# Kernel tuning notes

Measured on AMD Instinct MI355X. Metric: run time of the kernel, lower is better.

The kernel has to match this reference:

```python
import jax, jax.numpy as jnp
import numpy as np

WH, WW = 7, 7
SH, SW = 3, 3
NUM_HEADS = 8


def _rel_pos_index(wh, ww):
    coords = np.stack(np.meshgrid(np.arange(wh), np.arange(ww), indexing='ij')).reshape(2, -1)
    rel = (coords[:, :, None] - coords[:, None, :]).transpose(1, 2, 0)  # [N,N,2]
    rel[..., 0] += wh - 1
    rel[..., 1] += ww - 1
    rel[..., 0] *= 2 * ww - 1
    return rel.sum(-1)  # [N,N] int


def _attn_mask(Hp, Wp, wh, ww, sh, sw):
    img = np.zeros((Hp, Wp), dtype=np.float32)
    cnt = 0
    for hs in (slice(0, -wh), slice(-wh, -sh), slice(-sh, None)):
        for ws in (slice(0, -ww), slice(-ww, -sw), slice(-sw, None)):
            img[hs, ws] = cnt
            cnt += 1
    win = img.reshape(Hp // wh, wh, Wp // ww, ww).transpose(0, 2, 1, 3).reshape(-1, wh * ww)  # [nW,N]
    diff = win[:, None, :] - win[:, :, None]  # [nW,N,N]
    return np.where(diff != 0, -100.0, 0.0).astype(np.float32)


def _layernorm(x, g, b, eps=1e-5):
    mu = jnp.mean(x, -1, keepdims=True)
    var = jnp.mean(jnp.square(x - mu), -1, keepdims=True)
    return (x - mu) * jax.lax.rsqrt(var + eps) * g + b


def setup_inputs() -> dict:
    key = jax.random.key(0)
    ks = jax.random.split(key, 12)
    B, H, W, C = 32, 56, 56, 256
    hid = 4 * C
    s = lambda k, *shape: jax.random.normal(k, shape, jnp.float32) * 0.02
    return {
        'x': jax.random.normal(ks[0], (B, H * W, C), jnp.float32),
        'g1': jnp.ones((C,), jnp.float32), 'b1': jnp.zeros((C,), jnp.float32),
        'qkv_w': s(ks[1], 3 * C, C), 'qkv_b': jnp.zeros((3 * C,), jnp.float32),
        'bias_table': s(ks[2], (2 * WH - 1) * (2 * WW - 1), NUM_HEADS),
        'proj_w': s(ks[3], C, C), 'proj_b': jnp.zeros((C,), jnp.float32),
        'g2': jnp.ones((C,), jnp.float32), 'b2': jnp.zeros((C,), jnp.float32),
        'w1': s(ks[4], hid, C), 'bm1': jnp.zeros((hid,), jnp.float32),
        'w2': s(ks[5], C, hid), 'bm2': jnp.zeros((C,), jnp.float32),
        'H': H, 'W': W,
    }


def reference(x, g1, b1, qkv_w, qkv_b, bias_table, proj_w, proj_b, g2, b2, w1, bm1, w2, bm2, H, W):
    B, L, C = x.shape
    wh, ww = WH, WW
    nH = NUM_HEADS
    hd = C // nH
    scale = hd ** -0.5
    N = wh * ww

    shortcut = x
    h = _layernorm(x, g1, b1).reshape(B, H, W, C)
    pad_b = (wh - H % wh) % wh
    pad_r = (ww - W % ww) % ww
    if pad_b or pad_r:
        h = jnp.pad(h, ((0, 0), (0, pad_b), (0, pad_r), (0, 0)))
    Hp, Wp = h.shape[1], h.shape[2]

    h = jnp.roll(h, (-SH, -SW), axis=(1, 2))
    # window partition -> [B*nW, N, C]
    nWh, nWw = Hp // wh, Wp // ww
    xw = h.reshape(B, nWh, wh, nWw, ww, C).transpose(0, 1, 3, 2, 4, 5).reshape(-1, N, C)

    qkv = jnp.einsum('bnc,oc->bno', xw, qkv_w) + qkv_b  # [B*nW, N, 3C]
    qkv = qkv.reshape(-1, N, 3, nH, hd).transpose(2, 0, 3, 1, 4)
    q, k, v = qkv[0] * scale, qkv[1], qkv[2]  # [B*nW, nH, N, hd]
    attn = jnp.einsum('whnd,whmd->whnm', q, k)  # [B*nW, nH, N, N]

    rpi = jnp.asarray(_rel_pos_index(wh, ww))
    bias = bias_table[rpi.reshape(-1)].reshape(N, N, nH).transpose(2, 0, 1)  # [nH,N,N]
    attn = attn + bias[None]

    mask = jnp.asarray(_attn_mask(Hp, Wp, wh, ww, SH, SW))  # [nW,N,N]
    nW = mask.shape[0]
    attn = attn.reshape(B, nW, nH, N, N) + mask[None, :, None]
    attn = jax.nn.softmax(attn.reshape(-1, nH, N, N), axis=-1)

    out = jnp.einsum('whnm,whmd->whnd', attn, v).transpose(0, 2, 1, 3).reshape(-1, N, C)
    out = jnp.einsum('bnc,oc->bno', out, proj_w) + proj_b

    # window reverse
    out = out.reshape(B, nWh, nWw, wh, ww, C).transpose(0, 1, 3, 2, 4, 5).reshape(B, Hp, Wp, C)
    out = jnp.roll(out, (SH, SW), axis=(1, 2))
    if pad_b or pad_r:
        out = out[:, :H, :W, :]
    out = out.reshape(B, H * W, C)

    x = shortcut + out
    m = _layernorm(x, g2, b2)
    m = jax.nn.gelu(jnp.einsum('blc,oc->blo', m, w1) + bm1, approximate=False)
    m = jnp.einsum('blh,oh->blo', m, w2) + bm2
    return x + m
```

## Files before the change

kernel.cpp:

```cpp
#include <hip/hip_runtime.h>
#include <hip/hip_bf16.h>

#define DEVI __device__ __forceinline__
#define AS1 __attribute__((address_space(1)))
#define AS3 __attribute__((address_space(3)))

typedef short bf16x8 __attribute__((ext_vector_type(8)));
typedef float f32x4  __attribute__((ext_vector_type(4)));
typedef unsigned short u16x4 __attribute__((ext_vector_type(4)));

constexpr int MROWS = 100352;

DEVI int win_row_to_token(int r) {
  int b   = r / 3136;
  int rem = r - b * 3136;
  int wi  = rem / 49;
  int t   = rem - wi * 49;
  int nwh = wi >> 3, nww = wi & 7;
  int th = t / 7, tw = t - th * 7;
  int h = nwh * 7 + th + 3; if (h >= 56) h -= 56;
  int w = nww * 7 + tw + 3; if (w >= 56) w -= 56;
  return b * 3136 + h * 56 + w;
}

DEVI unsigned short f2bf(float f) {
  __hip_bfloat16 h = __float2bfloat16(f);
  return __builtin_bit_cast(unsigned short, h);
}

__global__ void pack_kernel(const float* __restrict__ W, __hip_bfloat16* __restrict__ Wp,
                            int N, int K) {
  long t = (long)blockIdx.x * 256 + threadIdx.x;
  long total = (long)N * K / 8;
  if (t >= total) return;
  int l  = (int)(t & 63);
  long f = t >> 6;
  int ni = (int)(f & 3);
  int kk = (int)((f >> 2) & 7);
  long r = f >> 5;
  int KB = K / 256;
  int kb = (int)(r % KB);
  int nb = (int)(r / KB);
  int row  = nb * 64 + (l & 15) + ni * 16;
  int col0 = kb * 256 + kk * 32 + (l >> 4) * 8;
  const float* src = W + (size_t)row * K + col0;
  u16x4 lo, hi;
  #pragma unroll
  for (int e = 0; e < 4; ++e) { lo[e] = f2bf(src[e]); hi[e] = f2bf(src[4 + e]); }
  *(u16x4*)(Wp + t * 8)     = lo;
  *(u16x4*)(Wp + t * 8 + 4) = hi;
}

template<bool WIN>
__global__ __launch_bounds__(256) void ln_kernel(
    const float* __restrict__ xin, const float* __restrict__ g,
    const float* __restrict__ b, __hip_bfloat16* __restrict__ outb)
{
  int r = blockIdx.x * 4 + (threadIdx.x >> 6);
  int l = threadIdx.x & 63;
  int tok = WIN ? win_row_to_token(r) : r;
  float4 xv = *(const float4*)&xin[(size_t)tok * 256 + l * 4];
  float s = xv.x + xv.y + xv.z + xv.w;
  float q = xv.x * xv.x + xv.y * xv.y + xv.z * xv.z + xv.w * xv.w;
  #pragma unroll
  for (int off = 32; off; off >>= 1) { s += __shfl_xor(s, off); q += __shfl_xor(q, off); }
  float mu = s * (1.0f / 256.0f);
  float var = q * (1.0f / 256.0f) - mu * mu;
  float rs = rsqrtf(var + 1e-5f);
  float4 gv = *(const float4*)&g[l * 4];
  float4 bv = *(const float4*)&b[l * 4];
  ushort4 st;
  st.x = f2bf((xv.x - mu) * rs * gv.x + bv.x);
  st.y = f2bf((xv.y - mu) * rs * gv.y + bv.y);
  st.z = f2bf((xv.z - mu) * rs * gv.z + bv.z);
  st.w = f2bf((xv.w - mu) * rs * gv.w + bv.w);
  *(ushort4*)&outb[(size_t)r * 256 + l * 4] = st;
}

enum { EPI_QKV = 0, EPI_PROJ = 1, EPI_MLP1 = 2, EPI_MLP2 = 3 };

template<int EPI, int KTOT>
__global__ __launch_bounds__(256, 3) void gemmA(
    const __hip_bfloat16* __restrict__ A,
    const __hip_bfloat16* __restrict__ Wp,
    int CB,
    const float* __restrict__ bias,
    const float* __restrict__ xres,
    float* __restrict__ outf,
    __hip_bfloat16* __restrict__ outb)
{
  constexpr int NKB = KTOT / 256;
  constexpr int K2  = KTOT * 2;
  __shared__ __align__(16) __hip_bfloat16 Al[64 * 256];

  const int tid = threadIdx.x;
  const int w = tid >> 6, l = tid & 63;
  const int g = l >> 4, lm = l & 15;

  const int nwg = gridDim.x;
  int bswz = (blockIdx.x & 7) * (nwg >> 3) + (blockIdx.x >> 3);
  const int mt = bswz / CB;
  const int cb = bswz - mt * CB;

  const char* At = (const char*)A + (size_t)mt * 64 * K2;
  char* AlB = (char*)Al;

  const int r0  = tid >> 5;
  const int usw = ((tid & 31) ^ r0) << 4;
  const int lmx = lm & 7;
  const int arow = lm * 512;

  const __hip_bfloat16* WpB = Wp + (size_t)(cb * 4 + w) * NKB * 16384;
  const int colb = cb * 256 + w * 64 + g * 4;

  f32x4 acc[4][4];
  {
    f32x4 bias_v[4];
    #pragma unroll
    for (int ni = 0; ni < 4; ++ni) bias_v[ni] = *(const f32x4*)&bias[colb + ni * 16];
    #pragma unroll
    for (int mi = 0; mi < 4; ++mi)
      #pragma unroll
      for (int ni = 0; ni < 4; ++ni) acc[mi][ni] = bias_v[ni];
  }

  #pragma unroll
  for (int kb = 0; kb < NKB; ++kb) {
    if (NKB > 1 && kb) __syncthreads();
    #pragma unroll
    for (int j = 0; j < 8; ++j)
      __builtin_amdgcn_global_load_lds(
          (const AS1 void*)(At + (long)(j * 8 + r0) * K2 + usw + kb * 512),
          (AS3 void*)(AlB + j * 4096 + w * 1024), 16, 0, 0);
    asm volatile("s_waitcnt vmcnt(0)" ::: "memory");
    __syncthreads();

    const __hip_bfloat16* Wk = WpB + (size_t)kb * 16384;
    #pragma unroll
    for (int kk = 0; kk < 8; ++kk) {
      bf16x8 bf[4], af[4];
      #pragma unroll
      for (int ni = 0; ni < 4; ++ni)
        bf[ni] = *(const bf16x8*)(Wk + ((kk * 4 + ni) * 64 + l) * 8);
      #pragma unroll
      for (int mi = 0; mi < 4; ++mi)
        af[mi] = *(const bf16x8*)(AlB + arow + mi * 8192 +
                                  ((((kk << 2) | g) ^ lmx) << 4));
      #pragma unroll
      for (int mi = 0; mi < 4; ++mi)
        #pragma unroll
        for (int ni = 0; ni < 4; ++ni)
          acc[mi][ni] = __builtin_amdgcn_mfma_f32_16x16x32_bf16(
              bf[ni], af[mi], acc[mi][ni], 0, 0, 0);
    }
  }

  #pragma unroll
  for (int mi = 0; mi < 4; ++mi) {
    int grow = mt * 64 + mi * 16 + lm;
    if (EPI == EPI_QKV) {
      __hip_bfloat16* rp = outb + (size_t)grow * 768 + colb;
      #pragma unroll
      for (int ni = 0; ni < 4; ++ni) {
        u16x4 st = { f2bf(acc[mi][ni][0]), f2bf(acc[mi][ni][1]),
                     f2bf(acc[mi][ni][2]), f2bf(acc[mi][ni][3]) };
        *(u16x4*)(rp + ni * 16) = st;
      }
    } else if (EPI == EPI_PROJ) {
      int orow = win_row_to_token(grow);
      const f32x4* xr = (const f32x4*)(xres + (size_t)orow * 256 + colb);
      f32x4* op = (f32x4*)(outf + (size_t)orow * 256 + colb);
      #pragma unroll
      for (int ni = 0; ni < 4; ++ni)
        op[ni * 4] = xr[ni * 4] + acc[mi][ni];
    } else if (EPI == EPI_MLP1) {
      __hip_bfloat16* rp = outb + (size_t)grow * 1024 + colb;
      #pragma unroll
      for (int ni = 0; ni < 4; ++ni) {
        u16x4 st;
        #pragma unroll
        for (int j = 0; j < 4; ++j) {
          float v = acc[mi][ni][j];
          float u2 = v * (1.5957691216f + 0.1426930877f * v * v);
          float e  = __expf(u2);
          st[j] = f2bf(v * e / (e + 1.0f));
        }
        *(u16x4*)(rp + ni * 16) = st;
      }
    } else {
      f32x4* op = (f32x4*)(outf + (size_t)grow * 256 + colb);
      #pragma unroll
      for (int ni = 0; ni < 4; ++ni)
        op[ni * 4] = op[ni * 4] + acc[mi][ni];
    }
  }
}

__global__ __launch_bounds__(256) void bias_prep_kernel(
    const float* __restrict__ bt, float* __restrict__ Sadd)
{
  int blk = blockIdx.x;
  int cls = blk >> 3, h = blk & 7;
  int re = cls >> 1, ce = cls & 1;
  int lane = threadIdx.x & 63, fs = threadIdx.x >> 6;
  int g = lane >> 4, lm = lane & 15;
  #pragma unroll
  for (int i = 0; i < 4; ++i) {
    int f = fs * 4 + i;
    int mi = f >> 2, ni = f & 3;
    int key = ni * 16 + lm;
    f32x4 v;
    #pragma unroll
    for (int j = 0; j < 4; ++j) {
      int q = mi * 16 + g * 4 + j;
      float val;
      if (key >= 49) {
        val = -1e30f;
      } else {
        int qq = q > 48 ? 48 : q;
        int qh = qq / 7, qw = qq - qh * 7;
        int kh = key / 7, kw = key - kh * 7;
        int rpi = (qh - kh + 6) * 13 + (qw - kw + 6);
        val = bt[rpi * 8 + h];
        int rq = (re ? (qh < 4 ? 1 : 2) : 0) * 3 + (ce ? (qw < 4 ? 1 : 2) : 0);
        int rk = (re ? (kh < 4 ? 1 : 2) : 0) * 3 + (ce ? (kw < 4 ? 1 : 2) : 0);
        if (rq != rk) val -= 100.0f;
      }
      v[j] = val;
    }
    ((f32x4*)Sadd)[(blk * 16 + f) * 64 + lane] = v;
  }
}

__global__ __launch_bounds__(256) void attn_mfma_kernel(
    const __hip_bfloat16* __restrict__ qkv,
    const float* __restrict__ Sadd,
    __hip_bfloat16* __restrict__ attn_out)
{
  __shared__ __align__(16) __hip_bfloat16 Pl[4][64 * 72];
  int blk = blockIdx.x;
  int win = blk >> 1, half = blk & 1;
  int w = threadIdx.x >> 6, l = threadIdx.x & 63;
  int head = half * 4 + w;
  int g = l >> 4, lm = l & 15;
  int wi = win & 63;
  int cls = (((wi >> 3) == 7) ? 2 : 0) | (((wi & 7) == 7) ? 1 : 0);
  const __hip_bfloat16* base = qkv + (size_t)win * 49 * 768 + head * 32;

  bf16x8 aQ[4], bK[4];
  #pragma unroll
  for (int mi = 0; mi < 4; ++mi) {
    int q = mi * 16 + lm; if (q > 48) q = 48;
    aQ[mi] = *(const bf16x8*)(base + q * 768 + g * 8);
  }
  #pragma unroll
  for (int ni = 0; ni < 4; ++ni) {
    int k = ni * 16 + lm; if (k > 48) k = 48;
    bK[ni] = *(const bf16x8*)(base + 256 + k * 768 + g * 8);
  }
  f32x4 acc[4][4] = {};
  #pragma unroll
  for (int mi = 0; mi < 4; ++mi)
    #pragma unroll
    for (int ni = 0; ni < 4; ++ni)
      acc[mi][ni] = __builtin_amdgcn_mfma_f32_16x16x32_bf16(aQ[mi], bK[ni], acc[mi][ni], 0, 0, 0);

  const float scale = 0.17677669529663687f;
  const f32x4* Sb = (const f32x4*)Sadd + (size_t)(cls * 8 + head) * 16 * 64 + l;

  f32x4 rsum[4];
  __hip_bfloat16* P = Pl[w];
  #pragma unroll
  for (int mi = 0; mi < 4; ++mi) {
    #pragma unroll
    for (int ni = 0; ni < 4; ++ni) {
      f32x4 sv = Sb[(mi * 4 + ni) * 64];
      #pragma unroll
      for (int j = 0; j < 4; ++j) acc[mi][ni][j] = acc[mi][ni][j] * scale + sv[j];
    }
    f32x4 mx = acc[mi][0];
    #pragma unroll
    for (int ni = 1; ni < 4; ++ni)
      #pragma unroll
      for (int j = 0; j < 4; ++j) mx[j] = fmaxf(mx[j], acc[mi][ni][j]);
    #pragma unroll
    for (int msk = 1; msk < 16; msk <<= 1)
      #pragma unroll
      for (int j = 0; j < 4; ++j) mx[j] = fmaxf(mx[j], __shfl_xor(mx[j], msk));
    f32x4 sm = {};
    #pragma unroll
    for (int ni = 0; ni < 4; ++ni)
      #pragma unroll
      for (int j = 0; j < 4; ++j) {
        float e = __expf(acc[mi][ni][j] - mx[j]);
        acc[mi][ni][j] = e;
        sm[j] += e;
      }
    #pragma unroll
    for (int msk = 1; msk < 16; msk <<= 1)
      #pragma unroll
      for (int j = 0; j < 4; ++j) sm[j] += __shfl_xor(sm[j], msk);
    rsum[mi] = sm;
    #pragma unroll
    for (int ni = 0; ni < 4; ++ni)
      #pragma unroll
      for (int j = 0; j < 4; ++j) {
        int q = mi * 16 + g * 4 + j;
        int key = ni * 16 + lm;
        P[q * 72 + key] = __float2bfloat16(acc[mi][ni][j]);
      }
  }

  bf16x8 bV[2][2];
  #pragma unroll
  for (int s = 0; s < 2; ++s)
    #pragma unroll
    for (int n2 = 0; n2 < 2; ++n2) {
      bf16x8 vv;
      #pragma unroll
      for (int e = 0; e < 8; ++e) {
        int key = s * 32 + g * 8 + e; if (key > 48) key = 48;
        vv[e] = __builtin_bit_cast(short, base[512 + key * 768 + n2 * 16 + lm]);
      }
      bV[s][n2] = vv;
    }

  f32x4 o[4][2] = {};
  #pragma unroll
  for (int s = 0; s < 2; ++s)
    #pragma unroll
    for (int mi2 = 0; mi2 < 4; ++mi2) {
      bf16x8 aP = *(const bf16x8*)&P[(mi2 * 16 + lm) * 72 + s * 32 + g * 8];
      #pragma unroll
      for (int n2 = 0; n2 < 2; ++n2)
        o[mi2][n2] = __builtin_amdgcn_mfma_f32_16x16x32_bf16(aP, bV[s][n2], o[mi2][n2], 0, 0, 0);
    }

  #pragma unroll
  for (int mi2 = 0; mi2 < 4; ++mi2) {
    f32x4 li;
    #pragma unroll
    for (int j = 0; j < 4; ++j) li[j] = 1.0f / rsum[mi2][j];
    #pragma unroll
    for (int n2 = 0; n2 < 2; ++n2)
      #pragma unroll
      for (int j = 0; j < 4; ++j) {
        int q = mi2 * 16 + g * 4 + j;
        if (q < 49)
          attn_out[((size_t)win * 49 + q) * 256 + head * 32 + n2 * 16 + lm] =
              __float2bfloat16(o[mi2][n2][j] * li[j]);
      }
  }
}

extern "C" void kernel_launch(void* const* d_in, const int* in_sizes, int n_in,
                              void* d_out, int out_size, void* d_ws, size_t ws_size,
                              hipStream_t stream) {
  const float* x          = (const float*)d_in[0];
  const float* g1         = (const float*)d_in[1];
  const float* b1         = (const float*)d_in[2];
  const float* qkv_w      = (const float*)d_in[3];
  const float* qkv_b      = (const float*)d_in[4];
  const float* bias_table = (const float*)d_in[5];
  const float* proj_w     = (const float*)d_in[6];
  const float* proj_b     = (const float*)d_in[7];
  const float* g2         = (const float*)d_in[8];
  const float* b2         = (const float*)d_in[9];
  const float* w1         = (const float*)d_in[10];
  const float* bm1        = (const float*)d_in[11];
  const float* w2         = (const float*)d_in[12];
  const float* bm2        = (const float*)d_in[13];
  float* out = (float*)d_out;

  char* ws = (char*)d_ws;
  __hip_bfloat16* A_ln   = (__hip_bfloat16*)(ws);
  __hip_bfloat16* qkvb   = (__hip_bfloat16*)(ws + 51380224);
  __hip_bfloat16* attn_o = (__hip_bfloat16*)(ws + 205520896);
  __hip_bfloat16* hidden = qkvb;
  __hip_bfloat16* qkv_wb  = (__hip_bfloat16*)(ws + 256901120);
  __hip_bfloat16* proj_wb = qkv_wb + 196608;
  __hip_bfloat16* w1b     = proj_wb + 65536;
  __hip_bfloat16* w2b     = w1b + 262144;
  float* Sadd = (float*)(ws + 258473984);

  pack_kernel<<<(196608 / 8 + 255) / 256, 256, 0, stream>>>(qkv_w, qkv_wb, 768, 256);
  pack_kernel<<<(65536  / 8 + 255) / 256, 256, 0, stream>>>(proj_w, proj_wb, 256, 256);
  pack_kernel<<<(262144 / 8 + 255) / 256, 256, 0, stream>>>(w1, w1b, 1024, 256);
  pack_kernel<<<(262144 / 8 + 255) / 256, 256, 0, stream>>>(w2, w2b, 256, 1024);
  bias_prep_kernel<<<32, 256, 0, stream>>>(bias_table, Sadd);

  ln_kernel<true><<<MROWS / 4, 256, 0, stream>>>(x, g1, b1, A_ln);

  gemmA<EPI_QKV, 256><<<1568 * 3, 256, 0, stream>>>(
      A_ln, qkv_wb, 3, qkv_b, nullptr, nullptr, qkvb);

  attn_mfma_kernel<<<4096, 256, 0, stream>>>(qkvb, Sadd, attn_o);

  gemmA<EPI_PROJ, 256><<<1568 * 1, 256, 0, stream>>>(
      attn_o, proj_wb, 1, proj_b, x, out, nullptr);

  ln_kernel<false><<<MROWS / 4, 256, 0, stream>>>(out, g2, b2, A_ln);

  gemmA<EPI_MLP1, 256><<<1568 * 4, 256, 0, stream>>>(
      A_ln, w1b, 4, bm1, nullptr, nullptr, hidden);

  gemmA<EPI_MLP2, 1024><<<1568 * 1, 256, 0, stream>>>(
      hidden, w2b, 1, bm2, nullptr, out, nullptr);
}
```

Baseline: 488.4 us.

## Fuse LayerNorm2 into proj GEMM and fuse MLP GEMMs with LDS-resident hidden

The proj GEMM epilogue now computes the residual sum and the second LayerNorm with a cross-wave LDS reduction, writing bf16 normalized rows directly and removing the standalone LN pass. The two MLP GEMMs become one kernel: each 64-row tile computes a 256-column hidden chunk, applies GELU, stages it in LDS and immediately accumulates it into the second GEMM. This avoids writing and re-reading the large bf16 hidden activation through global memory. In exchange the fused MLP kernel uses twice the LDS, runs at lower occupancy (launch bound 2), and has fewer blocks with serialized work per block.

```diff
diff --git a/kernel.cpp b/kernel.cpp
--- a/kernel.cpp
+++ b/kernel.cpp
@@ -26,6 +26,12 @@
 DEVI unsigned short f2bf(float f) {
   __hip_bfloat16 h = __float2bfloat16(f);
   return __builtin_bit_cast(unsigned short, h);
+}
+
+DEVI float gelu_t(float v) {
+  float u2 = v * (1.5957691216f + 0.1426930877f * v * v);
+  float e  = __expf(u2);
+  return v * e / (e + 1.0f);
 }
 
 __global__ void pack_kernel(const float* __restrict__ W, __hip_bfloat16* __restrict__ Wp,
@@ -51,14 +57,13 @@
   *(u16x4*)(Wp + t * 8 + 4) = hi;
 }
 
-template<bool WIN>
 __global__ __launch_bounds__(256) void ln_kernel(
     const float* __restrict__ xin, const float* __restrict__ g,
     const float* __restrict__ b, __hip_bfloat16* __restrict__ outb)
 {
   int r = blockIdx.x * 4 + (threadIdx.x >> 6);
   int l = threadIdx.x & 63;
-  int tok = WIN ? win_row_to_token(r) : r;
+  int tok = win_row_to_token(r);
   float4 xv = *(const float4*)&xin[(size_t)tok * 256 + l * 4];
   float s = xv.x + xv.y + xv.z + xv.w;
   float q = xv.x * xv.x + xv.y * xv.y + xv.z * xv.z + xv.w * xv.w;
@@ -77,20 +82,13 @@
   *(ushort4*)&outb[(size_t)r * 256 + l * 4] = st;
 }
 
-enum { EPI_QKV = 0, EPI_PROJ = 1, EPI_MLP1 = 2, EPI_MLP2 = 3 };
-
-template<int EPI, int KTOT>
-__global__ __launch_bounds__(256, 3) void gemmA(
+__global__ __launch_bounds__(256, 3) void gemm_qkv(
     const __hip_bfloat16* __restrict__ A,
     const __hip_bfloat16* __restrict__ Wp,
-    int CB,
     const float* __restrict__ bias,
-    const float* __restrict__ xres,
-    float* __restrict__ outf,
     __hip_bfloat16* __restrict__ outb)
 {
-  constexpr int NKB = KTOT / 256;
-  constexpr int K2  = KTOT * 2;
+  constexpr int CB = 3;
   __shared__ __align__(16) __hip_bfloat16 Al[64 * 256];
 
   const int tid = threadIdx.x;
@@ -102,15 +100,14 @@
   const int mt = bswz / CB;
   const int cb = bswz - mt * CB;
 
-  const char* At = (const char*)A + (size_t)mt * 64 * K2;
+  const char* At = (const char*)A + (size_t)mt * 64 * 512;
   char* AlB = (char*)Al;
-
   const int r0  = tid >> 5;
   const int usw = ((tid & 31) ^ r0) << 4;
   const int lmx = lm & 7;
   const int arow = lm * 512;
 
-  const __hip_bfloat16* WpB = Wp + (size_t)(cb * 4 + w) * NKB * 16384;
+  const __hip_bfloat16* WpB = Wp + (size_t)(cb * 4 + w) * 16384;
   const int colb = cb * 256 + w * 64 + g * 4;
 
   f32x4 acc[4][4];
@@ -125,74 +122,269 @@
   }
 
   #pragma unroll
-  for (int kb = 0; kb < NKB; ++kb) {
-    if (NKB > 1 && kb) __syncthreads();
-    #pragma unroll
-    for (int j = 0; j < 8; ++j)
-      __builtin_amdgcn_global_load_lds(
-          (const AS1 void*)(At + (long)(j * 8 + r0) * K2 + usw + kb * 512),
-          (AS3 void*)(AlB + j * 4096 + w * 1024), 16, 0, 0);
-    asm volatile("s_waitcnt vmcnt(0)" ::: "memory");
-    __syncthreads();
-
-    const __hip_bfloat16* Wk = WpB + (size_t)kb * 16384;
+  for (int j = 0; j < 8; ++j)
+    __builtin_amdgcn_global_load_lds(
+        (const AS1 void*)(At + (long)(j * 8 + r0) * 512 + usw),
+        (AS3 void*)(AlB + j * 4096 + w * 1024), 16, 0, 0);
+  asm volatile("s_waitcnt vmcnt(0)" ::: "memory");
+  __syncthreads();
+
+  #pragma unroll
+  for (int kk = 0; kk < 8; ++kk) {
+    bf16x8 bf[4], af[4];
+    #pragma unroll
+    for (int ni = 0; ni < 4; ++ni)
+      bf[ni] = *(const bf16x8*)(WpB + ((kk * 4 + ni) * 64 + l) * 8);
+    #pragma unroll
+    for (int mi = 0; mi < 4; ++mi)
+      af[mi] = *(const bf16x8*)(AlB + arow + mi * 8192 + ((((kk << 2) | g) ^ lmx) << 4));
+    #pragma unroll
+    for (int mi = 0; mi < 4; ++mi)
+      #pragma unroll
+      for (int ni = 0; ni < 4; ++ni)
+        acc[mi][ni] = __builtin_amdgcn_mfma_f32_16x16x32_bf16(bf[ni], af[mi], acc[mi][ni], 0, 0, 0);
+  }
+
+  #pragma unroll
+  for (int mi = 0; mi < 4; ++mi) {
+    int grow = mt * 64 + mi * 16 + lm;
+    __hip_bfloat16* rp = outb + (size_t)grow * 768 + colb;
+    #pragma unroll
+    for (int ni = 0; ni < 4; ++ni) {
+      u16x4 st = { f2bf(acc[mi][ni][0]), f2bf(acc[mi][ni][1]),
+                   f2bf(acc[mi][ni][2]), f2bf(acc[mi][ni][3]) };
+      *(u16x4*)(rp + ni * 16) = st;
+    }
+  }
+}
+
+__global__ __launch_bounds__(256, 3) void proj_ln2(
+    const __hip_bfloat16* __restrict__ A,
+    const __hip_bfloat16* __restrict__ Wp,
+    const float* __restrict__ bias,
+    const float* __restrict__ xres,
+    const float* __restrict__ g2, const float* __restrict__ b2,
+    float* __restrict__ outf,
+    __hip_bfloat16* __restrict__ alnout)
+{
+  __shared__ __align__(16) __hip_bfloat16 Al[64 * 256];
+  __shared__ float2 Sst[4][16][4];
+
+  const int tid = threadIdx.x;
+  const int w = tid >> 6, l = tid & 63;
+  const int g = l >> 4, lm = l & 15;
+
+  const int nwg = gridDim.x;
+  int bswz = (blockIdx.x & 7) * (nwg >> 3) + (blockIdx.x >> 3);
+  const int mt = bswz;
+
+  const char* At = (const char*)A + (size_t)mt * 64 * 512;
+  char* AlB = (char*)Al;
+  const int r0  = tid >> 5;
+  const int usw = ((tid & 31) ^ r0) << 4;
+  const int lmx = lm & 7;
+  const int arow = lm * 512;
+
+  const __hip_bfloat16* WpB = Wp + (size_t)w * 16384;
+  const int colb = w * 64 + g * 4;
+
+  f32x4 acc[4][4];
+  {
+    f32x4 bias_v[4];
+    #pragma unroll
+    for (int ni = 0; ni < 4; ++ni) bias_v[ni] = *(const f32x4*)&bias[colb + ni * 16];
+    #pragma unroll
+    for (int mi = 0; mi < 4; ++mi)
+      #pragma unroll
+      for (int ni = 0; ni < 4; ++ni) acc[mi][ni] = bias_v[ni];
+  }
+
+  #pragma unroll
+  for (int j = 0; j < 8; ++j)
+    __builtin_amdgcn_global_load_lds(
+        (const AS1 void*)(At + (long)(j * 8 + r0) * 512 + usw),
+        (AS3 void*)(AlB + j * 4096 + w * 1024), 16, 0, 0);
+  asm volatile("s_waitcnt vmcnt(0)" ::: "memory");
+  __syncthreads();
+
+  #pragma unroll
+  for (int kk = 0; kk < 8; ++kk) {
+    bf16x8 bf[4], af[4];
+    #pragma unroll
+    for (int ni = 0; ni < 4; ++ni)
+      bf[ni] = *(const bf16x8*)(WpB + ((kk * 4 + ni) * 64 + l) * 8);
+    #pragma unroll
+    for (int mi = 0; mi < 4; ++mi)
+      af[mi] = *(const bf16x8*)(AlB + arow + mi * 8192 + ((((kk << 2) | g) ^ lmx) << 4));
+    #pragma unroll
+    for (int mi = 0; mi < 4; ++mi)
+      #pragma unroll
+      for (int ni = 0; ni < 4; ++ni)
+        acc[mi][ni] = __builtin_amdgcn_mfma_f32_16x16x32_bf16(bf[ni], af[mi], acc[mi][ni], 0, 0, 0);
+  }
+
+  int orow_[4];
+  #pragma unroll
+  for (int mi = 0; mi < 4; ++mi) {
+    int grow = mt * 64 + mi * 16 + lm;
+    int orow = win_row_to_token(grow);
+    orow_[mi] = orow;
+    const f32x4* xr = (const f32x4*)(xres + (size_t)orow * 256 + colb);
+    f32x4* op = (f32x4*)(outf + (size_t)orow * 256 + colb);
+    float s = 0.0f, sq = 0.0f;
+    #pragma unroll
+    for (int ni = 0; ni < 4; ++ni) {
+      f32x4 r = xr[ni * 4] + acc[mi][ni];
+      acc[mi][ni] = r;
+      op[ni * 4] = r;
+      #pragma unroll
+      for (int j = 0; j < 4; ++j) { s += r[j]; sq += r[j] * r[j]; }
+    }
+    s  += __shfl_xor(s, 16);  sq += __shfl_xor(sq, 16);
+    s  += __shfl_xor(s, 32);  sq += __shfl_xor(sq, 32);
+    if (g == 0) Sst[mi][lm][w] = float2{s, sq};
+  }
+  __syncthreads();
+
+  f32x4 g2v[4], b2v[4];
+  #pragma unroll
+  for (int ni = 0; ni < 4; ++ni) {
+    g2v[ni] = *(const f32x4*)&g2[colb + ni * 16];
+    b2v[ni] = *(const f32x4*)&b2[colb + ni * 16];
+  }
+  #pragma unroll
+  for (int mi = 0; mi < 4; ++mi) {
+    float s = 0.0f, sq = 0.0f;
+    #pragma unroll
+    for (int ww = 0; ww < 4; ++ww) { float2 t = Sst[mi][lm][ww]; s += t.x; sq += t.y; }
+    float mu = s * (1.0f / 256.0f);
+    float rs = rsqrtf(sq * (1.0f / 256.0f) - mu * mu + 1e-5f);
+    __hip_bfloat16* ap = alnout + (size_t)orow_[mi] * 256 + colb;
+    #pragma unroll
+    for (int ni = 0; ni < 4; ++ni) {
+      u16x4 st;
+      #pragma unroll
+      for (int j = 0; j < 4; ++j)
+        st[j] = f2bf((acc[mi][ni][j] - mu) * rs * g2v[ni][j] + b2v[ni][j]);
+      *(u16x4*)(ap + ni * 16) = st;
+    }
+  }
+}
+
+__global__ __launch_bounds__(256, 2) void mlp_fused(
+    const __hip_bfloat16* __restrict__ A,
+    const __hip_bfloat16* __restrict__ W1p,
+    const __hip_bfloat16* __restrict__ W2p,
+    const float* __restrict__ bm1, const float* __restrict__ bm2,
+    float* __restrict__ outf)
+{
+  __shared__ __align__(16) __hip_bfloat16 Al[64 * 256];
+  __shared__ __align__(16) __hip_bfloat16 Hl[64 * 256];
+
+  const int tid = threadIdx.x;
+  const int w = tid >> 6, l = tid & 63;
+  const int g = l >> 4, lm = l & 15;
+
+  const int nwg = gridDim.x;
+  int bswz = (blockIdx.x & 7) * (nwg >> 3) + (blockIdx.x >> 3);
+  const int mt = bswz;
+
+  const char* At = (const char*)A + (size_t)mt * 64 * 512;
+  char* AlB = (char*)Al;
+  char* HlB = (char*)Hl;
+  const int r0  = tid >> 5;
+  const int usw = ((tid & 31) ^ r0) << 4;
+  const int lmx = lm & 7;
+  const int arow = lm * 512;
+  const int colb = w * 64 + g * 4;
+
+  #pragma unroll
+  for (int j = 0; j < 8; ++j)
+    __builtin_amdgcn_global_load_lds(
+        (const AS1 void*)(At + (long)(j * 8 + r0) * 512 + usw),
+        (AS3 void*)(AlB + j * 4096 + w * 1024), 16, 0, 0);
+  asm volatile("s_waitcnt vmcnt(0)" ::: "memory");
+  __syncthreads();
+
+  f32x4 acc2[4][4];
+  {
+    f32x4 b2v[4];
+    #pragma unroll
+    for (int ni = 0; ni < 4; ++ni) b2v[ni] = *(const f32x4*)&bm2[colb + ni * 16];
+    #pragma unroll
+    for (int mi = 0; mi < 4; ++mi)
+      #pragma unroll
+      for (int ni = 0; ni < 4; ++ni) acc2[mi][ni] = b2v[ni];
+  }
+
+  #pragma unroll
+  for (int q = 0; q < 4; ++q) {
+    f32x4 acc1[4][4];
+    {
+      f32x4 b1v[4];
+      #pragma unroll
+      for (int ni = 0; ni < 4; ++ni) b1v[ni] = *(const f32x4*)&bm1[q * 256 + colb + ni * 16];
+      #pragma unroll
+      for (int mi = 0; mi < 4; ++mi)
+        #pragma unroll
+        for (int ni = 0; ni < 4; ++ni) acc1[mi][ni] = b1v[ni];
+    }
+    const __hip_bfloat16* Wk1 = W1p + (size_t)(q * 4 + w) * 16384;
     #pragma unroll
     for (int kk = 0; kk < 8; ++kk) {
       bf16x8 bf[4], af[4];
       #pragma unroll
       for (int ni = 0; ni < 4; ++ni)
-        bf[ni] = *(const bf16x8*)(Wk + ((kk * 4 + ni) * 64 + l) * 8);
+        bf[ni] = *(const bf16x8*)(Wk1 + ((kk * 4 + ni) * 64 + l) * 8);
       #pragma unroll
       for (int mi = 0; mi < 4; ++mi)
-        af[mi] = *(const bf16x8*)(AlB + arow + mi * 8192 +
-                                  ((((kk << 2) | g) ^ lmx) << 4));
+        af[mi] = *(const bf16x8*)(AlB + arow + mi * 8192 + ((((kk << 2) | g) ^ lmx) << 4));
       #pragma unroll
       for (int mi = 0; mi < 4; ++mi)
         #pragma unroll
         for (int ni = 0; ni < 4; ++ni)
-          acc[mi][ni] = __builtin_amdgcn_mfma_f32_16x16x32_bf16(
-              bf[ni], af[mi], acc[mi][ni], 0, 0, 0);
+          acc1[mi][ni] = __builtin_amdgcn_mfma_f32_16x16x32_bf16(bf[ni], af[mi], acc1[mi][ni], 0, 0, 0);
+    }
+
+    __syncthreads();
+    #pragma unroll
+    for (int mi = 0; mi < 4; ++mi) {
+      int rowb = (mi * 16 + lm) * 512;
+      #pragma unroll
+      for (int ni = 0; ni < 4; ++ni) {
+        u16x4 hv = { f2bf(gelu_t(acc1[mi][ni][0])), f2bf(gelu_t(acc1[mi][ni][1])),
+                     f2bf(gelu_t(acc1[mi][ni][2])), f2bf(gelu_t(acc1[mi][ni][3])) };
+        int unit = (w * 8 + ni * 2 + (g >> 1)) ^ lmx;
+        *(u16x4*)(HlB + rowb + unit * 16 + (g & 1) * 8) = hv;
+      }
+    }
+    __syncthreads();
+
+    const __hip_bfloat16* Wk2 = W2p + (size_t)(w * 4 + q) * 16384;
+    #pragma unroll
+    for (int kk = 0; kk < 8; ++kk) {
+      bf16x8 bf[4], af[4];
+      #pragma unroll
+      for (int ni = 0; ni < 4; ++ni)
+        bf[ni] = *(const bf16x8*)(Wk2 + ((kk * 4 + ni) * 64 + l) * 8);
+      #pragma unroll
+      for (int mi = 0; mi < 4; ++mi)
+        af[mi] = *(const bf16x8*)(HlB + arow + mi * 8192 + ((((kk << 2) | g) ^ lmx) << 4));
+      #pragma unroll
+      for (int mi = 0; mi < 4; ++mi)
+        #pragma unroll
+        for (int ni = 0; ni < 4; ++ni)
+          acc2[mi][ni] = __builtin_amdgcn_mfma_f32_16x16x32_bf16(bf[ni], af[mi], acc2[mi][ni], 0, 0, 0);
     }
   }
 
   #pragma unroll
   for (int mi = 0; mi < 4; ++mi) {
     int grow = mt * 64 + mi * 16 + lm;
-    if (EPI == EPI_QKV) {
-      __hip_bfloat16* rp = outb + (size_t)grow * 768 + colb;
-      #pragma unroll
-      for (int ni = 0; ni < 4; ++ni) {
-        u16x4 st = { f2bf(acc[mi][ni][0]), f2bf(acc[mi][ni][1]),
-                     f2bf(acc[mi][ni][2]), f2bf(acc[mi][ni][3]) };
-        *(u16x4*)(rp + ni * 16) = st;
-      }
-    } else if (EPI == EPI_PROJ) {
-      int orow = win_row_to_token(grow);
-      const f32x4* xr = (const f32x4*)(xres + (size_t)orow * 256 + colb);
-      f32x4* op = (f32x4*)(outf + (size_t)orow * 256 + colb);
-      #pragma unroll
-      for (int ni = 0; ni < 4; ++ni)
-        op[ni * 4] = xr[ni * 4] + acc[mi][ni];
-    } else if (EPI == EPI_MLP1) {
-      __hip_bfloat16* rp = outb + (size_t)grow * 1024 + colb;
-      #pragma unroll
-      for (int ni = 0; ni < 4; ++ni) {
-        u16x4 st;
-        #pragma unroll
-        for (int j = 0; j < 4; ++j) {
-          float v = acc[mi][ni][j];
-          float u2 = v * (1.5957691216f + 0.1426930877f * v * v);
-          float e  = __expf(u2);
-          st[j] = f2bf(v * e / (e + 1.0f));
-        }
-        *(u16x4*)(rp + ni * 16) = st;
-      }
-    } else {
-      f32x4* op = (f32x4*)(outf + (size_t)grow * 256 + colb);
-      #pragma unroll
-      for (int ni = 0; ni < 4; ++ni)
-        op[ni * 4] = op[ni * 4] + acc[mi][ni];
-    }
+    f32x4* op = (f32x4*)(outf + (size_t)grow * 256 + colb);
+    #pragma unroll
+    for (int ni = 0; ni < 4; ++ni)
+      op[ni * 4] = op[ni * 4] + acc2[mi][ni];
   }
 }
 
@@ -376,7 +568,6 @@
   __hip_bfloat16* A_ln   = (__hip_bfloat16*)(ws);
   __hip_bfloat16* qkvb   = (__hip_bfloat16*)(ws + 51380224);
   __hip_bfloat16* attn_o = (__hip_bfloat16*)(ws + 205520896);
-  __hip_bfloat16* hidden = qkvb;
   __hip_bfloat16* qkv_wb  = (__hip_bfloat16*)(ws + 256901120);
   __hip_bfloat16* proj_wb = qkv_wb + 196608;
   __hip_bfloat16* w1b     = proj_wb + 65536;
@@ -389,21 +580,13 @@
   pack_kernel<<<(262144 / 8 + 255) / 256, 256, 0, stream>>>(w2, w2b, 256, 1024);
   bias_prep_kernel<<<32, 256, 0, stream>>>(bias_table, Sadd);
 
-  ln_kernel<true><<<MROWS / 4, 256, 0, stream>>>(x, g1, b1, A_ln);
-
-  gemmA<EPI_QKV, 256><<<1568 * 3, 256, 0, stream>>>(
-      A_ln, qkv_wb, 3, qkv_b, nullptr, nullptr, qkvb);
+  ln_kernel<<<MROWS / 4, 256, 0, stream>>>(x, g1, b1, A_ln);
+
+  gemm_qkv<<<1568 * 3, 256, 0, stream>>>(A_ln, qkv_wb, qkv_b, qkvb);
 
   attn_mfma_kernel<<<4096, 256, 0, stream>>>(qkvb, Sadd, attn_o);
 
-  gemmA<EPI_PROJ, 256><<<1568 * 1, 256, 0, stream>>>(
-      attn_o, proj_wb, 1, proj_b, x, out, nullptr);
-
-  ln_kernel<false><<<MROWS / 4, 256, 0, stream>>>(out, g2, b2, A_ln);
-
-  gemmA<EPI_MLP1, 256><<<1568 * 4, 256, 0, stream>>>(
-      A_ln, w1b, 4, bm1, nullptr, nullptr, hidden);
-
-  gemmA<EPI_MLP2, 1024><<<1568 * 1, 256, 0, stream>>>(
-      hidden, w2b, 1, bm2, nullptr, out, nullptr);
-}
+  proj_ln2<<<1568, 256, 0, stream>>>(attn_o, proj_wb, proj_b, x, g2, b2, out, A_ln);
+
+  mlp_fused<<<1568, 256, 0, stream>>>(A_ln, w1b, w2b, bm1, bm2, out);
+}
```

Measured after the change: 457.6 us. 6.3% less time.
